# Kernel optimization log

Measured on AMD Instinct MI355X. Metric: run time of the kernel, lower is better.

Reference implementation:

```python
import jax, jax.numpy as jnp
import numpy as np

N = 50000    # nodes
E = 600000   # edges
H = 128      # hidden_dim
NF = 12      # n_features
L = 4        # n_layers
EPS = 1e-5   # LayerNorm eps


def setup_inputs() -> dict:
    key = jax.random.key(0)
    ks = jax.random.split(key, 32)

    def w(k, shape, fan_in):
        return (jax.random.normal(k, shape, jnp.float32) / np.float32(np.sqrt(fan_in)))

    inp = {
        "x": jax.random.normal(ks[0], (N, NF), jnp.float32),
        "edge_index": jax.random.randint(ks[1], (2, E), 0, N, dtype=jnp.int64),
        # encoder: Linear(NF,H) -> ReLU -> Linear(H,H)
        "enc_W1": w(ks[2], (NF, H), NF), "enc_b1": jnp.zeros((H,), jnp.float32),
        "enc_W2": w(ks[3], (H, H), H),   "enc_b2": jnp.zeros((H,), jnp.float32),
        # L residual SAGE blocks (PyG SAGEConv: lin_l on mean-aggr w/ bias, lin_r on self no bias)
        "lin_l_W": w(ks[4], (L, H, H), H), "lin_l_b": jnp.zeros((L, H), jnp.float32),
        "lin_r_W": w(ks[5], (L, H, H), H),
        "ln_g": jnp.ones((L, H), jnp.float32), "ln_b": jnp.zeros((L, H), jnp.float32),
        # disp head: H->H->H//2->3
        "dW1": w(ks[6], (H, H), H),      "db1": jnp.zeros((H,), jnp.float32),
        "dW2": w(ks[7], (H, H // 2), H), "db2": jnp.zeros((H // 2,), jnp.float32),
        "dW3": w(ks[8], (H // 2, 3), H // 2), "db3": jnp.zeros((3,), jnp.float32),
        # stress head: H->H->H//2->1
        "sW1": w(ks[9], (H, H), H),       "sb1": jnp.zeros((H,), jnp.float32),
        "sW2": w(ks[10], (H, H // 2), H), "sb2": jnp.zeros((H // 2,), jnp.float32),
        "sW3": w(ks[11], (H // 2, 1), H // 2), "sb3": jnp.zeros((1,), jnp.float32),
    }
    return inp


def reference(x, edge_index, enc_W1, enc_b1, enc_W2, enc_b2,
              lin_l_W, lin_l_b, lin_r_W, ln_g, ln_b,
              dW1, db1, dW2, db2, dW3, db3,
              sW1, sb1, sW2, sb2, sW3, sb3):
    src, dst = edge_index[0], edge_index[1]

    # linear load-scaling ratio from load columns [3:6]
    load_mag = jnp.linalg.norm(x[:, 3:6], axis=1)
    ratio = jnp.max(load_mag)

    # encoder MLP
    h = jnp.maximum(x @ enc_W1 + enc_b1, 0.0) @ enc_W2 + enc_b2  # [N, H]

    # in-degree for mean aggregation (clamped to 1 like PyG)
    deg = jax.ops.segment_sum(jnp.ones((E,), h.dtype), dst, num_segments=N)
    inv_deg = 1.0 / jnp.clip(deg, 1.0)[:, None]  # [N, 1]

    for l in range(L):
        # SAGEConv: mean of neighbor (src) features at dst, then lin_l(aggr) + lin_r(self)
        agg = jax.ops.segment_sum(h[src], dst, num_segments=N) * inv_deg  # [N, H]
        y = agg @ lin_l_W[l] + lin_l_b[l] + h @ lin_r_W[l]
        # LayerNorm over channels
        mu = jnp.mean(y, axis=-1, keepdims=True)
        var = jnp.var(y, axis=-1, keepdims=True)
        y = (y - mu) * jax.lax.rsqrt(var + EPS) * ln_g[l] + ln_b[l]
        # residual + ReLU
        h = h + jnp.maximum(y, 0.0)

    # heads
    d = jnp.maximum(h @ dW1 + db1, 0.0)
    d = jnp.maximum(d @ dW2 + db2, 0.0) @ dW3 + db3  # [N, 3]
    s = jnp.maximum(h @ sW1 + sb1, 0.0)
    s = jnp.maximum(s @ sW2 + sb2, 0.0) @ sW3 + sb3  # [N, 1]

    # linear_scaling = True
    d = d * ratio
    s = s * ratio
    return jnp.concatenate([d, s], axis=1)  # [N, 4]
```

## Files before the change

kernel.cpp:

```cpp
#include <hip/hip_runtime.h>
#include <hip/hip_bf16.h>

typedef __hip_bfloat16 bf16;
typedef short bf16x8 __attribute__((ext_vector_type(8)));
typedef float f32x4 __attribute__((ext_vector_type(4)));

#define CAP 40

__device__ __forceinline__ float2 bfpair(unsigned u){
  float2 r; r.x = __uint_as_float(u<<16); r.y = __uint_as_float(u & 0xffff0000u); return r;
}
__device__ __forceinline__ float bfu(unsigned short u){ return __uint_as_float(((unsigned)u)<<16); }
__device__ __forceinline__ unsigned f2bf(float f){
  unsigned u = __float_as_uint(f);
  return (u + 0x7fffu + ((u>>16)&1u)) >> 16;
}
__device__ __forceinline__ unsigned fpack(float a, float b){
  return (f2bf(b)<<16) | f2bf(a);
}
__device__ __forceinline__ int edge_is64(const int* e){
  return (e[1]==0) & (e[3]==0) & (e[5]==0);
}
__device__ __forceinline__ int edge_ld(const int* e, int is64, int idx){
  return e[is64 ? 2*idx : idx];
}

__global__ void k_pre(const float* __restrict__ x, const int* __restrict__ eidx,
                      unsigned* __restrict__ ratio, int* __restrict__ cnt,
                      int* __restrict__ csr,
                      int N, int E, int nbE,
                      const float* __restrict__ llW, const float* __restrict__ lrW,
                      const float* __restrict__ dW1, const float* __restrict__ sW1,
                      const float* __restrict__ dW2, const float* __restrict__ sW2,
                      const float* __restrict__ eW2,
                      unsigned short* __restrict__ WTs, unsigned short* __restrict__ WT1,
                      unsigned short* __restrict__ WT2, unsigned short* __restrict__ WE2){
  int b = (int)blockIdx.x;
  if(b < nbE){
    int e = b*256 + threadIdx.x;
    if(e>=E) return;
    int is64 = edge_is64(eidx);
    int d = edge_ld(eidx, is64, E+e);
    int s = edge_ld(eidx, is64, e);
    if((unsigned)d >= (unsigned)N) return;
    if((unsigned)s >= (unsigned)N) s = 0;
    int p = atomicAdd(&cnt[d], 1);
    if(p < CAP) csr[(size_t)d*CAP + p] = s;
    return;
  }
  if(b < nbE + 256){
    int i = (b-nbE)*256 + threadIdx.x;
    int stride = 256*256;
    float m = 0.f;
    for(; i<N; i+=stride){
      float a = x[(size_t)i*12+3];
      float bb = x[(size_t)i*12+4];
      float c = x[(size_t)i*12+5];
      m = fmaxf(m, sqrtf(a*a+bb*bb+c*c));
    }
    #pragma unroll
    for(int off=1; off<64; off<<=1) m = fmaxf(m, __shfl_xor(m, off));
    if((threadIdx.x & 63)==0) atomicMax(ratio, __float_as_uint(m));
    return;
  }
  int idx = (b - nbE - 256)*256 + threadIdx.x;
  int j = idx & 7;
  int lane = (idx>>3) & 63;
  int q = lane >> 4, p = lane & 15;
  if(idx < 131072){
    int nt = (idx>>9) & 7, ks = (idx>>12) & 7, l = (idx>>15) & 3;
    int k = ks*32 + q*8 + j, n = nt*16 + p;
    float v = (k<128) ? llW[(size_t)l*16384 + (size_t)k*128 + n]
                      : lrW[(size_t)l*16384 + (size_t)(k-128)*128 + n];
    WTs[idx] = (unsigned short)f2bf(v);
  } else if(idx < 163840){
    int i2 = idx - 131072;
    int nt = (i2>>9) & 15, ks = (i2>>13) & 3;
    int k = ks*32 + q*8 + j, n = nt*16 + p;
    float v = (n<128) ? dW1[(size_t)k*128 + n] : sW1[(size_t)k*128 + (n-128)];
    WT1[i2] = (unsigned short)f2bf(v);
  } else if(idx < 180224){
    int i2 = idx - 163840;
    int nt = (i2>>9) & 7, ks = (i2>>12) & 3;
    int k = ks*32 + q*8 + j, n = nt*16 + p;
    float v = (n<64) ? dW2[(size_t)k*64 + n] : sW2[(size_t)k*64 + (n-64)];
    WT2[i2] = (unsigned short)f2bf(v);
  } else if(idx < 196608){
    int i2 = idx - 180224;
    int nt = (i2>>9) & 7, ks = (i2>>12) & 3;
    int k = ks*32 + q*8 + j, n = nt*16 + p;
    WE2[i2] = (unsigned short)f2bf(eW2[(size_t)k*128 + n]);
  }
}

__global__ __launch_bounds__(256) void k_enc(
  const float* __restrict__ x,
  const float* __restrict__ W1, const float* __restrict__ b1,
  const unsigned short* __restrict__ WE2, const float* __restrict__ b2,
  bf16* __restrict__ h, int N)
{
  __shared__ float Xs[64][12];
  __shared__ float W1s[12][128];
  __shared__ float b1s[128];
  __shared__ __align__(16) unsigned short T1b[64][136];
  int tid = threadIdx.x;
  int tx = tid & 31, ty = tid >> 5;
  int rowBase = blockIdx.x*64;
  for(int idx=tid; idx<768; idx+=256){
    int r = idx/12, c = idx - r*12;
    int row = rowBase + r;
    Xs[r][c] = (row<N)? x[(size_t)row*12+c] : 0.f;
  }
  for(int idx=tid; idx<1536; idx+=256) W1s[idx>>7][idx&127] = W1[idx];
  if(tid<128) b1s[tid] = b1[tid];
  __syncthreads();
  float acc[8][4] = {};
  #pragma unroll
  for(int k=0;k<12;k++){
    float4 w4 = *(float4*)&W1s[k][tx*4];
    #pragma unroll
    for(int r=0;r<8;r++){
      float a = Xs[ty*8+r][k];
      acc[r][0]+=a*w4.x; acc[r][1]+=a*w4.y; acc[r][2]+=a*w4.z; acc[r][3]+=a*w4.w;
    }
  }
  #pragma unroll
  for(int r=0;r<8;r++)
    #pragma unroll
    for(int c=0;c<4;c++)
      T1b[ty*8+r][tx*4+c] = (unsigned short)f2bf(fmaxf(acc[r][c] + b1s[tx*4+c], 0.f));
  __syncthreads();

  int lane = tid & 63;
  int w = tid >> 6, q = lane >> 4, p = lane & 15;
  f32x4 acc2[8];
  #pragma unroll
  for(int nt=0; nt<8; nt++) acc2[nt] = (f32x4){0.f,0.f,0.f,0.f};
  #pragma unroll
  for(int ks=0; ks<4; ks++){
    bf16x8 af = *(const bf16x8*)&T1b[w*16+p][ks*32+q*8];
    #pragma unroll
    for(int nt=0; nt<8; nt++){
      bf16x8 bfr = *(const bf16x8*)(WE2 + ((size_t)(ks*8+nt)*64 + lane)*8);
      acc2[nt] = __builtin_amdgcn_mfma_f32_16x16x32_bf16(af, bfr, acc2[nt], 0,0,0);
    }
  }
  float b2v[8];
  #pragma unroll
  for(int nt=0; nt<8; nt++) b2v[nt] = b2[nt*16+p];
  unsigned short* hu = (unsigned short*)h;
  #pragma unroll
  for(int r=0;r<4;r++){
    int row = rowBase + w*16 + q*4 + r;
    if(row < N){
      #pragma unroll
      for(int nt=0; nt<8; nt++)
        hu[(size_t)row*128 + nt*16+p] = (unsigned short)f2bf(acc2[nt][r] + b2v[nt]);
    }
  }
}

__global__ __launch_bounds__(256) void k_layer16(
    const bf16* __restrict__ hin, bf16* __restrict__ hout,
    const int* __restrict__ cnt, const int* __restrict__ csr,
    const unsigned short* __restrict__ WT,
    const float* __restrict__ bl, const float* __restrict__ lng,
    const float* __restrict__ lnb, int N)
{
  __shared__ __align__(16) unsigned short Ag[16][136];
  __shared__ float sPart[4][16];
  __shared__ float qPart[4][16];
  int tid = threadIdx.x;
  int rowBase = blockIdx.x*16;

  {
    int qw = tid >> 4;
    int l  = tid & 15;
    int row = rowBase + qw;
    float a0=0.f,a1=0.f,a2=0.f,a3=0.f,a4=0.f,a5=0.f,a6=0.f,a7=0.f;
    if(row < N){
      int dc = cnt[row]; if(dc > CAP) dc = CAP;
      const int* cp = csr + (size_t)row*CAP;
      int i = 0;
      for(; i+4<=dc; i+=4){
        int j0=cp[i], j1=cp[i+1], j2=cp[i+2], j3=cp[i+3];
        uint4 u0 = *(const uint4*)(hin + (size_t)j0*128 + l*8);
        uint4 u1 = *(const uint4*)(hin + (size_t)j1*128 + l*8);
        uint4 u2 = *(const uint4*)(hin + (size_t)j2*128 + l*8);
        uint4 u3 = *(const uint4*)(hin + (size_t)j3*128 + l*8);
        float2 f;
        f=bfpair(u0.x); a0+=f.x; a1+=f.y;  f=bfpair(u0.y); a2+=f.x; a3+=f.y;
        f=bfpair(u0.z); a4+=f.x; a5+=f.y;  f=bfpair(u0.w); a6+=f.x; a7+=f.y;
        f=bfpair(u1.x); a0+=f.x; a1+=f.y;  f=bfpair(u1.y); a2+=f.x; a3+=f.y;
        f=bfpair(u1.z); a4+=f.x; a5+=f.y;  f=bfpair(u1.w); a6+=f.x; a7+=f.y;
        f=bfpair(u2.x); a0+=f.x; a1+=f.y;  f=bfpair(u2.y); a2+=f.x; a3+=f.y;
        f=bfpair(u2.z); a4+=f.x; a5+=f.y;  f=bfpair(u2.w); a6+=f.x; a7+=f.y;
        f=bfpair(u3.x); a0+=f.x; a1+=f.y;  f=bfpair(u3.y); a2+=f.x; a3+=f.y;
        f=bfpair(u3.z); a4+=f.x; a5+=f.y;  f=bfpair(u3.w); a6+=f.x; a7+=f.y;
      }
      for(; i<dc; ++i){
        int jj = cp[i];
        uint4 u = *(const uint4*)(hin + (size_t)jj*128 + l*8);
        float2 f;
        f=bfpair(u.x); a0+=f.x; a1+=f.y;  f=bfpair(u.y); a2+=f.x; a3+=f.y;
        f=bfpair(u.z); a4+=f.x; a5+=f.y;  f=bfpair(u.w); a6+=f.x; a7+=f.y;
      }
      float id = 1.0f / (float)(dc>0? dc : 1);
      a0*=id; a1*=id; a2*=id; a3*=id; a4*=id; a5*=id; a6*=id; a7*=id;
    }
    uint4 o;
    o.x = fpack(a0,a1); o.y = fpack(a2,a3);
    o.z = fpack(a4,a5); o.w = fpack(a6,a7);
    *(uint4*)&Ag[qw][l*8] = o;
  }
  __syncthreads();

  int lane = tid & 63;
  int w = tid >> 6;
  int q = lane >> 4;
  int p = lane & 15;
  int nt0 = 2*w, nt1 = 2*w+1;
  int am = rowBase + p;
  bool ok = am < N;
  const unsigned short* hRow = (const unsigned short*)hin + (size_t)am*128;

  f32x4 accA = (f32x4){0.f,0.f,0.f,0.f};
  f32x4 accB = (f32x4){0.f,0.f,0.f,0.f};
  #pragma unroll
  for(int ks=0; ks<8; ks++){
    bf16x8 af;
    if(ks < 4){
      af = *(const bf16x8*)&Ag[p][ks*32 + q*8];
    } else {
      af = (bf16x8){0,0,0,0,0,0,0,0};
      if(ok) af = *(const bf16x8*)(hRow + (ks-4)*32 + q*8);
    }
    bf16x8 b0 = *(const bf16x8*)(WT + ((size_t)(ks*8+nt0)*64 + lane)*8);
    bf16x8 b1 = *(const bf16x8*)(WT + ((size_t)(ks*8+nt1)*64 + lane)*8);
    accA = __builtin_amdgcn_mfma_f32_16x16x32_bf16(af, b0, accA, 0,0,0);
    accB = __builtin_amdgcn_mfma_f32_16x16x32_bf16(af, b1, accB, 0,0,0);
  }

  int c0 = nt0*16 + p, c1 = nt1*16 + p;
  float bl0 = bl[c0], g0 = lng[c0], lb0 = lnb[c0];
  float bl1 = bl[c1], g1 = lng[c1], lb1 = lnb[c1];
  float y0[4], y1[4];
  #pragma unroll
  for(int r=0;r<4;r++){
    y0[r] = accA[r] + bl0;
    y1[r] = accB[r] + bl1;
    float s  = y0[r] + y1[r];
    float sq = y0[r]*y0[r] + y1[r]*y1[r];
    #pragma unroll
    for(int off=1; off<16; off<<=1){ s += __shfl_xor(s, off); sq += __shfl_xor(sq, off); }
    if(p==0){ sPart[w][q*4+r] = s; qPart[w][q*4+r] = sq; }
  }
  __syncthreads();

  const unsigned short* hiu = (const unsigned short*)hin;
  unsigned short* hou = (unsigned short*)hout;
  #pragma unroll
  for(int r=0;r<4;r++){
    int rloc = q*4 + r;
    float s  = sPart[0][rloc]+sPart[1][rloc]+sPart[2][rloc]+sPart[3][rloc];
    float sq = qPart[0][rloc]+qPart[1][rloc]+qPart[2][rloc]+qPart[3][rloc];
    float mu = s*(1.f/128.f);
    float var = fmaxf(sq*(1.f/128.f) - mu*mu, 0.f);
    float rstd = rsqrtf(var + 1e-5f);
    int row = rowBase + rloc;
    if(row < N){
      float h0 = bfu(hiu[(size_t)row*128 + c0]);
      float h1 = bfu(hiu[(size_t)row*128 + c1]);
      float o0 = h0 + fmaxf((y0[r]-mu)*rstd*g0 + lb0, 0.f);
      float o1 = h1 + fmaxf((y1[r]-mu)*rstd*g1 + lb1, 0.f);
      hou[(size_t)row*128 + c0] = (unsigned short)f2bf(o0);
      hou[(size_t)row*128 + c1] = (unsigned short)f2bf(o1);
    }
  }
}

__global__ __launch_bounds__(256) void k_heads_mfma(
  const bf16* __restrict__ h,
  const unsigned short* __restrict__ WT1,
  const unsigned short* __restrict__ WT2,
  const float* __restrict__ db1, const float* __restrict__ sb1,
  const float* __restrict__ db2, const float* __restrict__ sb2,
  const float* __restrict__ dW3, const float* __restrict__ db3,
  const float* __restrict__ sW3, const float* __restrict__ sb3,
  const float* __restrict__ ratio_p, float* __restrict__ out, int N)
{
  __shared__ __align__(16) unsigned short T1s[4][16][264];
  const float ratio = *ratio_p;
  int tid = threadIdx.x;
  int lane = tid & 63;
  int w = tid >> 6;
  int q = lane >> 4;
  int p = lane & 15;
  int rowBase = blockIdx.x*64;
  int am = rowBase + w*16 + p;
  bool arow_ok = am < N;
  const unsigned short* hRow = (const unsigned short*)h + (size_t)am*128;

  f32x4 acc1[16];
  #pragma unroll
  for(int nt=0; nt<16; nt++) acc1[nt] = (f32x4){0.f,0.f,0.f,0.f};
  #pragma unroll
  for(int ks=0; ks<4; ks++){
    int koff = ks*32 + q*8;
    bf16x8 af = {0,0,0,0,0,0,0,0};
    if(arow_ok) af = *(const bf16x8*)(hRow + koff);
    #pragma unroll
    for(int nt=0; nt<16; nt++){
      bf16x8 bfr = *(const bf16x8*)(WT1 + ((size_t)(ks*16+nt)*64 + lane)*8);
      acc1[nt] = __builtin_amdgcn_mfma_f32_16x16x32_bf16(af, bfr, acc1[nt], 0,0,0);
    }
  }
  #pragma unroll
  for(int nt=0; nt<16; nt++){
    float b1v = (nt<8) ? db1[nt*16+p] : sb1[(nt-8)*16+p];
    #pragma unroll
    for(int r=0;r<4;r++){
      float v = fmaxf(acc1[nt][r] + b1v, 0.f);
      T1s[w][q*4+r][nt*16+p] = (unsigned short)f2bf(v);
    }
  }
  __syncthreads();

  f32x4 acc2[8];
  #pragma unroll
  for(int nt=0; nt<8; nt++) acc2[nt] = (f32x4){0.f,0.f,0.f,0.f};
  #pragma unroll
  for(int ks=0; ks<4; ks++){
    int koff = ks*32 + q*8;
    bf16x8 ad = *(const bf16x8*)&T1s[w][p][koff];
    bf16x8 as = *(const bf16x8*)&T1s[w][p][128+koff];
    #pragma unroll
    for(int nt=0; nt<8; nt++){
      bf16x8 bfr = *(const bf16x8*)(WT2 + ((size_t)(ks*8+nt)*64 + lane)*8);
      acc2[nt] = __builtin_amdgcn_mfma_f32_16x16x32_bf16(nt<4? ad : as, bfr, acc2[nt], 0,0,0);
    }
  }

  float w3d[4][3], w3s[4], bd2[4], bs2[4];
  #pragma unroll
  for(int nt=0; nt<4; nt++){
    #pragma unroll
    for(int c=0;c<3;c++) w3d[nt][c] = dW3[(nt*16+p)*3 + c];
    w3s[nt] = sW3[nt*16+p];
    bd2[nt] = db2[nt*16+p];
    bs2[nt] = sb2[nt*16+p];
  }
  float b3v = (p==0)? db3[0] : (p==1)? db3[1] : (p==2)? db3[2] : sb3[0];
  #pragma unroll
  for(int r=0;r<4;r++){
    int row = rowBase + w*16 + q*4 + r;
    float pd0=0.f, pd1=0.f, pd2=0.f, ps=0.f;
    #pragma unroll
    for(int nt=0; nt<4; nt++){
      float td = fmaxf(acc2[nt][r]   + bd2[nt], 0.f);
      float ts = fmaxf(acc2[nt+4][r] + bs2[nt], 0.f);
      pd0 += td*w3d[nt][0]; pd1 += td*w3d[nt][1]; pd2 += td*w3d[nt][2];
      ps  += ts*w3s[nt];
    }
    #pragma unroll
    for(int off=1; off<16; off<<=1){
      pd0 += __shfl_xor(pd0, off); pd1 += __shfl_xor(pd1, off);
      pd2 += __shfl_xor(pd2, off); ps  += __shfl_xor(ps, off);
    }
    if(row < N && p < 4){
      float v = (p==0)? pd0 : (p==1)? pd1 : (p==2)? pd2 : ps;
      out[(size_t)row*4 + p] = (v + b3v)*ratio;
    }
  }
}

extern "C" void kernel_launch(void* const* d_in, const int* in_sizes, int n_in,
                              void* d_out, int out_size, void* d_ws, size_t ws_size,
                              hipStream_t stream)
{
  const float* x   = (const float*)d_in[0];
  const int*  eidx = (const int*) d_in[1];
  const float* eW1 = (const float*)d_in[2];
  const float* eb1 = (const float*)d_in[3];
  const float* eW2 = (const float*)d_in[4];
  const float* eb2 = (const float*)d_in[5];
  const float* llW = (const float*)d_in[6];
  const float* llb = (const float*)d_in[7];
  const float* lrW = (const float*)d_in[8];
  const float* lng = (const float*)d_in[9];
  const float* lnb = (const float*)d_in[10];
  const float* dW1 = (const float*)d_in[11];
  const float* db1 = (const float*)d_in[12];
  const float* dW2 = (const float*)d_in[13];
  const float* db2 = (const float*)d_in[14];
  const float* dW3 = (const float*)d_in[15];
  const float* db3 = (const float*)d_in[16];
  const float* sW1 = (const float*)d_in[17];
  const float* sb1 = (const float*)d_in[18];
  const float* sW2 = (const float*)d_in[19];
  const float* sb2 = (const float*)d_in[20];
  const float* sW3 = (const float*)d_in[21];
  const float* sb3 = (const float*)d_in[22];
  float* out = (float*)d_out;

  const int N = in_sizes[0] / 12;
  const int E = in_sizes[1] / 2;
  (void)n_in; (void)out_size; (void)ws_size;

  char* base = (char*)d_ws;
  size_t off = 0;
  auto alloc = [&](size_t nbytes)->char*{
    char* p = base + off; off += (nbytes + 255) & ~(size_t)255; return p;
  };
  unsigned* ratio = (unsigned*)alloc(4);
  int*   cnt    = (int*)  alloc((size_t)N*4);
  int*   csr    = (int*)  alloc((size_t)N*CAP*4);
  bf16*  hA     = (bf16*) alloc((size_t)N*128*2);
  bf16*  hB     = (bf16*) alloc((size_t)N*128*2);
  unsigned short* WTs  = (unsigned short*)alloc((size_t)131072*2);
  unsigned short* WT1h = (unsigned short*)alloc((size_t)32768*2);
  unsigned short* WT2h = (unsigned short*)alloc((size_t)16384*2);
  unsigned short* WE2  = (unsigned short*)alloc((size_t)16384*2);

  size_t zbytes = (size_t)((char*)csr - base);
  hipMemsetAsync(d_ws, 0, zbytes, stream);

  int nbE    = (E + 255)/256;
  int nbTile = (N + 63)/64;
  int nbLay  = (N + 15)/16;

  k_pre  <<<nbE + 256 + 768, 256, 0, stream>>>(x, eidx, ratio, cnt, csr, N, E, nbE,
      llW, lrW, dW1, sW1, dW2, sW2, eW2, WTs, WT1h, WT2h, WE2);
  k_enc  <<<nbTile, 256, 0, stream>>>(x, eW1, eb1, WE2, eb2, hA, N);

  bf16* hin = hA; bf16* hout = hB;
  for(int l=0;l<4;l++){
    k_layer16<<<nbLay, 256, 0, stream>>>(hin, hout, cnt, csr,
        WTs + (size_t)l*32768,
        llb + (size_t)l*128, lng + (size_t)l*128, lnb + (size_t)l*128, N);
    bf16* t = hin; hin = hout; hout = t;
  }
  k_heads_mfma<<<nbTile, 256, 0, stream>>>(hin, WT1h, WT2h,
      db1, sb1, db2, sb2, dW3, db3, sW3, sb3, (const float*)ratio, out, N);
}
```

Baseline: 322.4 us.

## Merge CSR build into encoder kernel and widen neighbor gather unroll

```diff
diff --git a/kernel.cpp b/kernel.cpp
--- a/kernel.cpp
+++ b/kernel.cpp
@@ -25,31 +25,17 @@
   return e[is64 ? 2*idx : idx];
 }
 
-__global__ void k_pre(const float* __restrict__ x, const int* __restrict__ eidx,
-                      unsigned* __restrict__ ratio, int* __restrict__ cnt,
-                      int* __restrict__ csr,
-                      int N, int E, int nbE,
-                      const float* __restrict__ llW, const float* __restrict__ lrW,
-                      const float* __restrict__ dW1, const float* __restrict__ sW1,
-                      const float* __restrict__ dW2, const float* __restrict__ sW2,
-                      const float* __restrict__ eW2,
-                      unsigned short* __restrict__ WTs, unsigned short* __restrict__ WT1,
-                      unsigned short* __restrict__ WT2, unsigned short* __restrict__ WE2){
+__global__ __launch_bounds__(256) void k_swz(
+    const float* __restrict__ x, unsigned* __restrict__ ratio,
+    const float* __restrict__ llW, const float* __restrict__ lrW,
+    const float* __restrict__ dW1, const float* __restrict__ sW1,
+    const float* __restrict__ dW2, const float* __restrict__ sW2,
+    const float* __restrict__ eW2,
+    unsigned short* __restrict__ WTs, unsigned short* __restrict__ WT1,
+    unsigned short* __restrict__ WT2, unsigned short* __restrict__ WE2, int N){
   int b = (int)blockIdx.x;
-  if(b < nbE){
-    int e = b*256 + threadIdx.x;
-    if(e>=E) return;
-    int is64 = edge_is64(eidx);
-    int d = edge_ld(eidx, is64, E+e);
-    int s = edge_ld(eidx, is64, e);
-    if((unsigned)d >= (unsigned)N) return;
-    if((unsigned)s >= (unsigned)N) s = 0;
-    int p = atomicAdd(&cnt[d], 1);
-    if(p < CAP) csr[(size_t)d*CAP + p] = s;
-    return;
-  }
-  if(b < nbE + 256){
-    int i = (b-nbE)*256 + threadIdx.x;
+  if(b >= 768){
+    int i = (b-768)*256 + threadIdx.x;
     int stride = 256*256;
     float m = 0.f;
     for(; i<N; i+=stride){
@@ -63,7 +49,7 @@
     if((threadIdx.x & 63)==0) atomicMax(ratio, __float_as_uint(m));
     return;
   }
-  int idx = (b - nbE - 256)*256 + threadIdx.x;
+  int idx = b*256 + threadIdx.x;
   int j = idx & 7;
   int lane = (idx>>3) & 63;
   int q = lane >> 4, p = lane & 15;
@@ -85,7 +71,7 @@
     int k = ks*32 + q*8 + j, n = nt*16 + p;
     float v = (n<64) ? dW2[(size_t)k*64 + n] : sW2[(size_t)k*64 + (n-64)];
     WT2[i2] = (unsigned short)f2bf(v);
-  } else if(idx < 196608){
+  } else {
     int i2 = idx - 180224;
     int nt = (i2>>9) & 7, ks = (i2>>12) & 3;
     int k = ks*32 + q*8 + j, n = nt*16 + p;
@@ -93,19 +79,50 @@
   }
 }
 
-__global__ __launch_bounds__(256) void k_enc(
-  const float* __restrict__ x,
+__global__ __launch_bounds__(256) void k_main(
+  const float* __restrict__ x, const int* __restrict__ eidx,
+  int* __restrict__ cnt, int* __restrict__ csr,
   const float* __restrict__ W1, const float* __restrict__ b1,
   const unsigned short* __restrict__ WE2, const float* __restrict__ b2,
-  bf16* __restrict__ h, int N)
+  bf16* __restrict__ h, int N, int E, int nbE4)
 {
+  int b = (int)blockIdx.x;
+  if(b < nbE4){
+    int is64 = edge_is64(eidx);
+    int e0 = b*1024 + threadIdx.x;
+    int e1 = e0+256, e2 = e0+512, e3 = e0+768;
+    int s0=0,s1=0,s2=0,s3=0,d0=0,d1=0,d2=0,d3=0;
+    bool v0 = e0<E, v1 = e1<E, v2 = e2<E, v3 = e3<E;
+    if(v0){ d0=edge_ld(eidx,is64,E+e0); s0=edge_ld(eidx,is64,e0); }
+    if(v1){ d1=edge_ld(eidx,is64,E+e1); s1=edge_ld(eidx,is64,e1); }
+    if(v2){ d2=edge_ld(eidx,is64,E+e2); s2=edge_ld(eidx,is64,e2); }
+    if(v3){ d3=edge_ld(eidx,is64,E+e3); s3=edge_ld(eidx,is64,e3); }
+    v0 = v0 && (unsigned)d0 < (unsigned)N;
+    v1 = v1 && (unsigned)d1 < (unsigned)N;
+    v2 = v2 && (unsigned)d2 < (unsigned)N;
+    v3 = v3 && (unsigned)d3 < (unsigned)N;
+    if((unsigned)s0 >= (unsigned)N) s0 = 0;
+    if((unsigned)s1 >= (unsigned)N) s1 = 0;
+    if((unsigned)s2 >= (unsigned)N) s2 = 0;
+    if((unsigned)s3 >= (unsigned)N) s3 = 0;
+    int p0=-1,p1=-1,p2=-1,p3=-1;
+    if(v0) p0 = atomicAdd(&cnt[d0], 1);
+    if(v1) p1 = atomicAdd(&cnt[d1], 1);
+    if(v2) p2 = atomicAdd(&cnt[d2], 1);
+    if(v3) p3 = atomicAdd(&cnt[d3], 1);
+    if(v0 && p0 < CAP) csr[(size_t)d0*CAP + p0] = s0;
+    if(v1 && p1 < CAP) csr[(size_t)d1*CAP + p1] = s1;
+    if(v2 && p2 < CAP) csr[(size_t)d2*CAP + p2] = s2;
+    if(v3 && p3 < CAP) csr[(size_t)d3*CAP + p3] = s3;
+    return;
+  }
   __shared__ float Xs[64][12];
   __shared__ float W1s[12][128];
   __shared__ float b1s[128];
   __shared__ __align__(16) unsigned short T1b[64][136];
   int tid = threadIdx.x;
   int tx = tid & 31, ty = tid >> 5;
-  int rowBase = blockIdx.x*64;
+  int rowBase = (b - nbE4)*64;
   for(int idx=tid; idx<768; idx+=256){
     int r = idx/12, c = idx - r*12;
     int row = rowBase + r;
@@ -182,21 +199,34 @@
       int dc = cnt[row]; if(dc > CAP) dc = CAP;
       const int* cp = csr + (size_t)row*CAP;
       int i = 0;
-      for(; i+4<=dc; i+=4){
-        int j0=cp[i], j1=cp[i+1], j2=cp[i+2], j3=cp[i+3];
-        uint4 u0 = *(const uint4*)(hin + (size_t)j0*128 + l*8);
-        uint4 u1 = *(const uint4*)(hin + (size_t)j1*128 + l*8);
-        uint4 u2 = *(const uint4*)(hin + (size_t)j2*128 + l*8);
-        uint4 u3 = *(const uint4*)(hin + (size_t)j3*128 + l*8);
-        float2 f;
-        f=bfpair(u0.x); a0+=f.x; a1+=f.y;  f=bfpair(u0.y); a2+=f.x; a3+=f.y;
-        f=bfpair(u0.z); a4+=f.x; a5+=f.y;  f=bfpair(u0.w); a6+=f.x; a7+=f.y;
-        f=bfpair(u1.x); a0+=f.x; a1+=f.y;  f=bfpair(u1.y); a2+=f.x; a3+=f.y;
-        f=bfpair(u1.z); a4+=f.x; a5+=f.y;  f=bfpair(u1.w); a6+=f.x; a7+=f.y;
-        f=bfpair(u2.x); a0+=f.x; a1+=f.y;  f=bfpair(u2.y); a2+=f.x; a3+=f.y;
-        f=bfpair(u2.z); a4+=f.x; a5+=f.y;  f=bfpair(u2.w); a6+=f.x; a7+=f.y;
-        f=bfpair(u3.x); a0+=f.x; a1+=f.y;  f=bfpair(u3.y); a2+=f.x; a3+=f.y;
-        f=bfpair(u3.z); a4+=f.x; a5+=f.y;  f=bfpair(u3.w); a6+=f.x; a7+=f.y;
+      for(; i+8<=dc; i+=8){
+        uint4 u[8];
+        #pragma unroll
+        for(int t=0;t<8;t++){
+          int jj = cp[i+t];
+          u[t] = *(const uint4*)(hin + (size_t)jj*128 + l*8);
+        }
+        #pragma unroll
+        for(int t=0;t<8;t++){
+          float2 f;
+          f=bfpair(u[t].x); a0+=f.x; a1+=f.y;  f=bfpair(u[t].y); a2+=f.x; a3+=f.y;
+          f=bfpair(u[t].z); a4+=f.x; a5+=f.y;  f=bfpair(u[t].w); a6+=f.x; a7+=f.y;
+        }
+      }
+      if(i+4<=dc){
+        uint4 u[4];
+        #pragma unroll
+        for(int t=0;t<4;t++){
+          int jj = cp[i+t];
+          u[t] = *(const uint4*)(hin + (size_t)jj*128 + l*8);
+        }
+        #pragma unroll
+        for(int t=0;t<4;t++){
+          float2 f;
+          f=bfpair(u[t].x); a0+=f.x; a1+=f.y;  f=bfpair(u[t].y); a2+=f.x; a3+=f.y;
+          f=bfpair(u[t].z); a4+=f.x; a5+=f.y;  f=bfpair(u[t].w); a6+=f.x; a7+=f.y;
+        }
+        i += 4;
       }
       for(; i<dc; ++i){
         int jj = cp[i];
@@ -425,13 +455,14 @@
   size_t zbytes = (size_t)((char*)csr - base);
   hipMemsetAsync(d_ws, 0, zbytes, stream);
 
-  int nbE    = (E + 255)/256;
+  int nbE4   = (E + 1023)/1024;
   int nbTile = (N + 63)/64;
   int nbLay  = (N + 15)/16;
 
-  k_pre  <<<nbE + 256 + 768, 256, 0, stream>>>(x, eidx, ratio, cnt, csr, N, E, nbE,
-      llW, lrW, dW1, sW1, dW2, sW2, eW2, WTs, WT1h, WT2h, WE2);
-  k_enc  <<<nbTile, 256, 0, stream>>>(x, eW1, eb1, WE2, eb2, hA, N);
+  k_swz <<<1024, 256, 0, stream>>>(x, ratio, llW, lrW, dW1, sW1, dW2, sW2, eW2,
+      WTs, WT1h, WT2h, WE2, N);
+  k_main<<<nbE4 + nbTile, 256, 0, stream>>>(x, eidx, cnt, csr,
+      eW1, eb1, WE2, eb2, hA, N, E, nbE4);
 
   bf16* hin = hA; bf16* hout = hB;
   for(int l=0;l<4;l++){
```

Result: slower. 354.8 us (+10.1%).
